# Performance work log

Hardware: AMD Instinct MI355X
Metric: run time of the kernel (lower is better)

## Reference

```python
import jax, jax.numpy as jnp
import numpy as np

N, DEG, F_IN, H = 50000, 16, 128, 32
E = N * DEG


def _linear_params(key, out_f, in_f):
    kw, kb = jax.random.split(key)
    s = 1.0 / np.sqrt(in_f)
    W = jax.random.uniform(kw, (out_f, in_f), jnp.float32, -s, s)
    b = jax.random.uniform(kb, (out_f,), jnp.float32, -s, s)
    return W, b


def setup_inputs() -> dict:
    key = jax.random.key(0)
    ks = jax.random.split(key, 12)
    X = jax.random.normal(ks[0], (N, F_IN), jnp.float32)
    # DEG distinct nonzero offsets shared by all rows -> unique (src,dst) pairs,
    # so the COO tensor is already coalesced (no duplicate indices).
    offsets = jax.random.permutation(ks[1], jnp.arange(1, N))[:DEG]
    src = jnp.repeat(jnp.arange(N, dtype=jnp.int32), DEG)
    dst = ((src.reshape(N, DEG) + offsets[None, :].astype(jnp.int32)) % N).reshape(-1)
    D = jax.ops.segment_sum(jnp.ones((E,), jnp.float32), src, num_segments=N)
    wn1p, bn1p = _linear_params(ks[2], H, F_IN)      # convN1.pass_map
    wn1s, bn1s = _linear_params(ks[3], H, F_IN)      # convN1.self_map
    we1p, be1p = _linear_params(ks[4], H, 2 * H)     # convE1.pass_map
    we1s, be1s = _linear_params(ks[5], H, F_IN)      # convE1.self_map
    wn2p, bn2p = _linear_params(ks[6], H, H)         # convN2.pass_map
    wn2s, bn2s = _linear_params(ks[7], H, H)         # convN2.self_map
    we2p, be2p = _linear_params(ks[8], H, 2 * H)     # convE2.pass_map
    we2s, be2s = _linear_params(ks[9], H, H)         # convE2.self_map
    wc, bc = _linear_params(ks[10], 1, H)            # classifier
    return dict(X=X, src=src, dst=dst, D=D,
                wn1p=wn1p, bn1p=bn1p, wn1s=wn1s, bn1s=bn1s,
                we1p=we1p, be1p=be1p, we1s=we1s, be1s=be1s,
                wn2p=wn2p, bn2p=bn2p, wn2s=wn2s, bn2s=bn2s,
                we2p=we2p, be2p=be2p, we2s=we2s, be2s=be2s,
                wc=wc, bc=bc)


def reference(X, src, dst, D,
              wn1p, bn1p, wn1s, bn1s,
              we1p, be1p, we1s, be1s,
              wn2p, bn2p, wn2s, bn2s,
              we2p, be2p, we2s, be2s,
              wc, bc):
    n = X.shape[0]

    def node_conv(vals, Xn, wp, bp, ws, bs):
        # torch.sparse.sum(A, dim=1): sum edge values per source row
        Asum = jax.ops.segment_sum(vals, src, num_segments=n)
        return jax.nn.relu((Asum / D[:, None]) @ wp.T + bp + Xn @ ws.T + bs)

    def edge_conv(vals, Xn, wp, bp, ws, bs):
        X1, X2 = Xn[src], Xn[dst]
        Ef = jnp.concatenate([(X1 - X2) * 0.5, (X1 + X2) * 0.5], axis=-1)
        return jax.nn.relu(Ef @ wp.T + bp + vals @ ws.T + bs)

    # add_graph: edge features = |X[src] - X[dst]|
    vals0 = jnp.abs(X[src] - X[dst])            # (E, F_IN)
    X0 = jnp.zeros_like(X)                       # forward zeros node features
    Xn1 = node_conv(vals0, X0, wn1p, bn1p, wn1s, bn1s)   # (N, 32)
    vals1 = edge_conv(vals0, Xn1, we1p, be1p, we1s, be1s)  # (E, 32)
    Xn2 = node_conv(vals1, Xn1, wn2p, bn2p, wn2s, bn2s)  # (N, 32)
    vals2 = edge_conv(vals1, Xn2, we2p, be2p, we2s, be2s)  # (E, 32)
    SX = jax.nn.sigmoid(vals2 @ wc.T + bc)[:, 0]          # (E,)
    return SX
```

## Files before the change

kernel.cpp:

```cpp
#include <hip/hip_runtime.h>

#define DEG 16
#define F_IN 128
#define H 32

typedef __attribute__((ext_vector_type(8))) _Float16 f16x8;
typedef __attribute__((ext_vector_type(4))) float f32x4;
typedef __attribute__((ext_vector_type(4))) int i32x4;
typedef __attribute__((ext_vector_type(4))) float fv4;
typedef __attribute__((ext_vector_type(2))) unsigned int uv2;

union HS  { _Float16 f; unsigned short s; };
union HF4 { _Float16 h[4]; uv2 u; };

__device__ __forceinline__ float relu_f(float x) { return fmaxf(x, 0.0f); }

__device__ __forceinline__ f16x8 habs8(f16x8 a) {
    union { f16x8 h; i32x4 i; } u; u.h = a;
#pragma unroll
    for (int k = 0; k < 4; ++k) u.i[k] &= 0x7FFF7FFF;
    return u.h;
}

__global__ __launch_bounds__(256) void k_pre(
    const float* __restrict__ X, _Float16* __restrict__ Xh, long n8,
    const float* __restrict__ we1s, const float* __restrict__ we1p,
    const float* __restrict__ be1p, const float* __restrict__ be1s,
    const float* __restrict__ we2p, const float* __restrict__ we2s,
    const float* __restrict__ be2p, const float* __restrict__ be2s,
    const float* __restrict__ wn1p, const float* __restrict__ bn1p,
    const float* __restrict__ bn1s,
    const float* __restrict__ wn2p, const float* __restrict__ bn2p,
    const float* __restrict__ wn2s, const float* __restrict__ bn2s,
    _Float16* __restrict__ Wcat1, _Float16* __restrict__ Wcat2,
    _Float16* __restrict__ Wn1ph,
    _Float16* __restrict__ Wn2ph, _Float16* __restrict__ Wn2sh,
    float* __restrict__ bias1, float* __restrict__ bias2,
    float* __restrict__ biasn1, float* __restrict__ biasn2)
{
    if (blockIdx.x >= 32) {
        const long t = (long)(blockIdx.x - 32) * 256 + threadIdx.x;
        if (t >= n8) return;
        const fv4* p = (const fv4*)X + t * 2;
        const fv4 a = __builtin_nontemporal_load(p);
        const fv4 b = __builtin_nontemporal_load(p + 1);
        f16x8 h;
        h[0] = (_Float16)a[0]; h[1] = (_Float16)a[1]; h[2] = (_Float16)a[2]; h[3] = (_Float16)a[3];
        h[4] = (_Float16)b[0]; h[5] = (_Float16)b[1]; h[6] = (_Float16)b[2]; h[7] = (_Float16)b[3];
        *(f16x8*)(Xh + t * 8) = h;
        return;
    }
    const int t0 = blockIdx.x * 256 + threadIdx.x;
    const int stride = 32 * 256;
    for (int idx = t0; idx < 32 * 192; idx += stride) {
        const int n = idx / 192, k = idx - n * 192;
        float w;
        if (k < 128)       w = we1s[n * 128 + k];
        else if (k < 160)  w = 0.5f * we1p[n * 64 + (k - 128)];
        else               w = 0.5f * we1p[n * 64 + 32 + (k - 160)];
        Wcat1[idx] = (_Float16)w;
    }
    for (int idx = t0; idx < 32 * 96; idx += stride) {
        const int n = idx / 96, k = idx - n * 96;
        float w;
        if (k < 32)       w = 0.5f * we2p[n * 64 + k];
        else if (k < 64)  w = 0.5f * we2p[n * 64 + 32 + (k - 32)];
        else              w = we2s[n * 32 + (k - 64)];
        Wcat2[idx] = (_Float16)w;
    }
    for (int idx = t0; idx < 32 * 128; idx += stride)
        Wn1ph[idx] = (_Float16)wn1p[idx];
    for (int idx = t0; idx < 32 * 32; idx += stride) {
        Wn2ph[idx] = (_Float16)wn2p[idx];
        Wn2sh[idx] = (_Float16)wn2s[idx];
    }
    if (t0 < H) {
        bias1[t0]  = be1p[t0] + be1s[t0];
        bias2[t0]  = be2p[t0] + be2s[t0];
        biasn1[t0] = bn1p[t0] + bn1s[t0];
        biasn2[t0] = bn2p[t0] + bn2s[t0];
    }
}

__global__ __launch_bounds__(64, 3) void k_p1(
    const _Float16* __restrict__ Xh, const int* __restrict__ dst,
    const float* __restrict__ D,
    const _Float16* __restrict__ Wcat1, const _Float16* __restrict__ Wn1ph,
    const float* __restrict__ biasn1,
    _Float16* __restrict__ t1h, _Float16* __restrict__ Xn1h, int N)
{
    const int lane = threadIdx.x;
    const int m = lane & 15, g = lane >> 4;
    const int i0 = blockIdx.x * 16;
    const int srow = (i0 + m < N) ? (i0 + m) : (N - 1);

    i32x4 dj4[4];
    {
        const i32x4* dp = (const i32x4*)(dst + (size_t)srow * DEG);
#pragma unroll
        for (int q = 0; q < 4; ++q) dj4[q] = dp[q];
    }
    f16x8 sv[4];
#pragma unroll
    for (int kb = 0; kb < 4; ++kb)
        sv[kb] = *(const f16x8*)(Xh + (size_t)srow * F_IN + kb * 32 + g * 8);
    f16x8 Bs[4][2], Bn[4][2];
#pragma unroll
    for (int kb = 0; kb < 4; ++kb)
#pragma unroll
        for (int t = 0; t < 2; ++t) {
            Bs[kb][t] = *(const f16x8*)(Wcat1 + (t * 16 + m) * 192 + kb * 32 + g * 8);
            Bn[kb][t] = *(const f16x8*)(Wn1ph + (t * 16 + m) * 128 + kb * 32 + g * 8);
        }

    f16x8 tvc[4], tvn[4];
#pragma unroll
    for (int kb = 0; kb < 4; ++kb)
        tvc[kb] = *(const f16x8*)(Xh + (size_t)dj4[0][0] * F_IN + kb * 32 + g * 8);

    f32x4 cn0 = {0.f,0.f,0.f,0.f}, cn1 = {0.f,0.f,0.f,0.f};
#pragma unroll
    for (int j = 0; j < 16; ++j) {
        if (j < 15) {
            const int dn = dj4[(j + 1) >> 2][(j + 1) & 3];
#pragma unroll
            for (int kb = 0; kb < 4; ++kb)
                tvn[kb] = *(const f16x8*)(Xh + (size_t)dn * F_IN + kb * 32 + g * 8);
        }
        f32x4 cs0 = {0.f,0.f,0.f,0.f}, cs1 = {0.f,0.f,0.f,0.f};
#pragma unroll
        for (int kb = 0; kb < 4; ++kb) {
            const f16x8 a = habs8(sv[kb] - tvc[kb]);
            cs0 = __builtin_amdgcn_mfma_f32_16x16x32_f16(a, Bs[kb][0], cs0, 0, 0, 0);
            cs1 = __builtin_amdgcn_mfma_f32_16x16x32_f16(a, Bs[kb][1], cs1, 0, 0, 0);
            cn0 = __builtin_amdgcn_mfma_f32_16x16x32_f16(a, Bn[kb][0], cn0, 0, 0, 0);
            cn1 = __builtin_amdgcn_mfma_f32_16x16x32_f16(a, Bn[kb][1], cn1, 0, 0, 0);
        }
        const size_t tb = ((size_t)blockIdx.x * 16 + j) * 512;
        HF4 a;
#pragma unroll
        for (int r = 0; r < 4; ++r) a.h[r] = (_Float16)cs0[r];
        __builtin_nontemporal_store(a.u, (uv2*)(t1h + tb + lane * 4));
#pragma unroll
        for (int r = 0; r < 4; ++r) a.h[r] = (_Float16)cs1[r];
        __builtin_nontemporal_store(a.u, (uv2*)(t1h + tb + 256 + lane * 4));
#pragma unroll
        for (int kb = 0; kb < 4; ++kb) tvc[kb] = tvn[kb];
    }
    const float bn0 = biasn1[m], bn1v = biasn1[16 + m];
#pragma unroll
    for (int r = 0; r < 4; ++r) {
        const int node = i0 + g * 4 + r;
        if (node < N) {
            const float invD = 1.0f / D[node];
            Xn1h[(size_t)node * H + m]      = (_Float16)relu_f(cn0[r] * invD + bn0);
            Xn1h[(size_t)node * H + 16 + m] = (_Float16)relu_f(cn1[r] * invD + bn1v);
        }
    }
}

__global__ __launch_bounds__(256, 4) void k_p2(
    const int* __restrict__ dst, const _Float16* __restrict__ Xn1h,
    const _Float16* __restrict__ Wcat1, const float* __restrict__ bias1,
    const _Float16* __restrict__ Wn2ph, const _Float16* __restrict__ Wn2sh,
    const float* __restrict__ biasn2, const float* __restrict__ D,
    _Float16* t1v1,
    _Float16* __restrict__ Xn2h, int N)
{
    __shared__ unsigned short RP[4][16 * 40];
    __shared__ float red[4][8][64];
    const int tid = threadIdx.x;
    const int lane = tid & 63;
    const int w = tid >> 6;
    const int m = lane & 15, g = lane >> 4;
    const int i0 = blockIdx.x * 16;
    const int srow = (i0 + m < N) ? (i0 + m) : (N - 1);

    const i32x4 dj = ((const i32x4*)(dst + (size_t)srow * DEG))[w];
    const f16x8 x1 = *(const f16x8*)(Xn1h + (size_t)srow * H + g * 8);
    f16x8 Bf[2][2];
#pragma unroll
    for (int kb = 0; kb < 2; ++kb)
#pragma unroll
        for (int t = 0; t < 2; ++t)
            Bf[kb][t] = *(const f16x8*)(Wcat1 + (t * 16 + m) * 192 + (4 + kb) * 32 + g * 8);

    f16x8 x2c, x2n;
    uv2 u0c, u1c, u0n, u1n;
    {
        const int d0 = dj[0];
        x2c = *(const f16x8*)(Xn1h + (size_t)d0 * H + g * 8);
        const size_t tb = ((size_t)blockIdx.x * 16 + w * 4) * 512;
        u0c = __builtin_nontemporal_load((const uv2*)(t1v1 + tb + lane * 4));
        u1c = __builtin_nontemporal_load((const uv2*)(t1v1 + tb + 256 + lane * 4));
    }
    const float b0 = bias1[m], b1v = bias1[16 + m];
    f32x4 sB0 = {0.f,0.f,0.f,0.f}, sB1 = {0.f,0.f,0.f,0.f};
    const int rr = lane >> 2, qq = lane & 3;
    unsigned short* RPw = RP[w];
#pragma unroll
    for (int jj = 0; jj < 4; ++jj) {
        if (jj < 3) {
            const int dn = dj[jj + 1];
            x2n = *(const f16x8*)(Xn1h + (size_t)dn * H + g * 8);
            const size_t tbn = ((size_t)blockIdx.x * 16 + w * 4 + jj + 1) * 512;
            u0n = __builtin_nontemporal_load((const uv2*)(t1v1 + tbn + lane * 4));
            u1n = __builtin_nontemporal_load((const uv2*)(t1v1 + tbn + 256 + lane * 4));
        }
        f32x4 c0, c1;
        { HF4 a; a.u = u0c;
#pragma unroll
          for (int r = 0; r < 4; ++r) c0[r] = (float)a.h[r];
          a.u = u1c;
#pragma unroll
          for (int r = 0; r < 4; ++r) c1[r] = (float)a.h[r]; }
        const f16x8 ad = x1 - x2c;
        const f16x8 aS = x1 + x2c;
        c0 = __builtin_amdgcn_mfma_f32_16x16x32_f16(ad, Bf[0][0], c0, 0, 0, 0);
        c1 = __builtin_amdgcn_mfma_f32_16x16x32_f16(ad, Bf[0][1], c1, 0, 0, 0);
        c0 = __builtin_amdgcn_mfma_f32_16x16x32_f16(aS, Bf[1][0], c0, 0, 0, 0);
        c1 = __builtin_amdgcn_mfma_f32_16x16x32_f16(aS, Bf[1][1], c1, 0, 0, 0);
#pragma unroll
        for (int r = 0; r < 4; ++r) {
            const float v0 = relu_f(c0[r] + b0);
            const float v1 = relu_f(c1[r] + b1v);
            HS h0, h1; h0.f = (_Float16)v0; h1.f = (_Float16)v1;
            RPw[(g * 4 + r) * 40 + m]      = h0.s;
            RPw[(g * 4 + r) * 40 + 16 + m] = h1.s;
            sB0[r] += v0; sB1[r] += v1;
        }
        const size_t tb = ((size_t)blockIdx.x * 16 + w * 4 + jj) * 512;
        const i32x4 v = *(const i32x4*)(RPw + rr * 40 + qq * 8);
        *(i32x4*)(t1v1 + tb + rr * 32 + qq * 8) = v;
        x2c = x2n; u0c = u0n; u1c = u1n;
    }
#pragma unroll
    for (int r = 0; r < 4; ++r) {
        red[w][r][lane]     = sB0[r];
        red[w][4 + r][lane] = sB1[r];
    }
    __syncthreads();
    if (w == 0) {
        _Float16* RPh = (_Float16*)RP[0];
#pragma unroll
        for (int r = 0; r < 4; ++r) {
            const int node = i0 + g * 4 + r;
            const float invD = 1.0f / D[(node < N) ? node : (N - 1)];
            const float a0 = red[0][r][lane] + red[1][r][lane]
                           + red[2][r][lane] + red[3][r][lane];
            const float a1 = red[0][4+r][lane] + red[1][4+r][lane]
                           + red[2][4+r][lane] + red[3][4+r][lane];
            RPh[(g * 4 + r) * 40 + m]      = (_Float16)(a0 * invD);
            RPh[(g * 4 + r) * 40 + 16 + m] = (_Float16)(a1 * invD);
        }
        const f16x8 aF = *(const f16x8*)(RPh + m * 40 + g * 8);
        f16x8 Bp[2], Bs2[2];
#pragma unroll
        for (int t = 0; t < 2; ++t) {
            Bp[t]  = *(const f16x8*)(Wn2ph + (t * 16 + m) * H + g * 8);
            Bs2[t] = *(const f16x8*)(Wn2sh + (t * 16 + m) * H + g * 8);
        }
        f32x4 c0 = {0.f,0.f,0.f,0.f}, c1 = {0.f,0.f,0.f,0.f};
        c0 = __builtin_amdgcn_mfma_f32_16x16x32_f16(aF, Bp[0], c0, 0, 0, 0);
        c1 = __builtin_amdgcn_mfma_f32_16x16x32_f16(aF, Bp[1], c1, 0, 0, 0);
        c0 = __builtin_amdgcn_mfma_f32_16x16x32_f16(x1, Bs2[0], c0, 0, 0, 0);
        c1 = __builtin_amdgcn_mfma_f32_16x16x32_f16(x1, Bs2[1], c1, 0, 0, 0);
        const float bp0 = biasn2[m], bp1 = biasn2[16 + m];
#pragma unroll
        for (int r = 0; r < 4; ++r) {
            const int node = i0 + g * 4 + r;
            if (node < N) {
                Xn2h[(size_t)node * H + m]      = (_Float16)relu_f(c0[r] + bp0);
                Xn2h[(size_t)node * H + 16 + m] = (_Float16)relu_f(c1[r] + bp1);
            }
        }
    }
}

__global__ __launch_bounds__(256, 4) void k_p3(
    const _Float16* __restrict__ Xn2h, const int* __restrict__ dst,
    const _Float16* __restrict__ vals1,
    const _Float16* __restrict__ Wcat2, const float* __restrict__ bias2,
    const float* __restrict__ wc, const float* __restrict__ bc,
    float* __restrict__ out, int N)
{
    __shared__ float outS[16 * 16];
    const int tid = threadIdx.x;
    const int lane = tid & 63;
    const int w = tid >> 6;
    const int m = lane & 15, g = lane >> 4;
    const int i0 = blockIdx.x * 16;
    const int srow = (i0 + m < N) ? (i0 + m) : (N - 1);

    const i32x4 dj = ((const i32x4*)(dst + (size_t)srow * DEG))[w];
    const f16x8 x1 = *(const f16x8*)(Xn2h + (size_t)srow * H + g * 8);
    f16x8 Bf[3][2];
#pragma unroll
    for (int kb = 0; kb < 3; ++kb)
#pragma unroll
        for (int t = 0; t < 2; ++t)
            Bf[kb][t] = *(const f16x8*)(Wcat2 + (t * 16 + m) * 96 + kb * 32 + g * 8);

    f16x8 x2b[2], avb[2];
#pragma unroll
    for (int s = 0; s < 2; ++s) {
        const int dn = dj[s];
        x2b[s] = *(const f16x8*)(Xn2h + (size_t)dn * H + g * 8);
        avb[s] = *(const f16x8*)(vals1 + ((size_t)blockIdx.x * 16 + w * 4 + s) * 512 + m * 32 + g * 8);
    }
    const float b0 = bias2[m], b1v = bias2[16 + m];
    const float w0 = wc[m], w1 = wc[16 + m];
#pragma unroll
    for (int jj = 0; jj < 4; ++jj) {
        const int s = jj & 1;
        const f16x8 x2 = x2b[s];
        const f16x8 av = avb[s];
        if (jj < 2) {
            const int dn = dj[jj + 2];
            x2b[s] = *(const f16x8*)(Xn2h + (size_t)dn * H + g * 8);
            avb[s] = *(const f16x8*)(vals1 + ((size_t)blockIdx.x * 16 + w * 4 + jj + 2) * 512 + m * 32 + g * 8);
        }
        const f16x8 ad = x1 - x2;
        const f16x8 aS = x1 + x2;
        f32x4 c0 = {0.f,0.f,0.f,0.f}, c1 = {0.f,0.f,0.f,0.f};
        c0 = __builtin_amdgcn_mfma_f32_16x16x32_f16(ad, Bf[0][0], c0, 0, 0, 0);
        c1 = __builtin_amdgcn_mfma_f32_16x16x32_f16(ad, Bf[0][1], c1, 0, 0, 0);
        c0 = __builtin_amdgcn_mfma_f32_16x16x32_f16(aS, Bf[1][0], c0, 0, 0, 0);
        c1 = __builtin_amdgcn_mfma_f32_16x16x32_f16(aS, Bf[1][1], c1, 0, 0, 0);
        c0 = __builtin_amdgcn_mfma_f32_16x16x32_f16(av, Bf[2][0], c0, 0, 0, 0);
        c1 = __builtin_amdgcn_mfma_f32_16x16x32_f16(av, Bf[2][1], c1, 0, 0, 0);

        float sr[4];
#pragma unroll
        for (int r = 0; r < 4; ++r)
            sr[r] = relu_f(c0[r] + b0) * w0 + relu_f(c1[r] + b1v) * w1;
#pragma unroll
        for (int mask = 1; mask < 16; mask <<= 1) {
#pragma unroll
            for (int r = 0; r < 4; ++r)
                sr[r] += __shfl_xor(sr[r], mask);
        }
        if (m == 0) {
#pragma unroll
            for (int r = 0; r < 4; ++r)
                outS[(g * 4 + r) * 16 + (w * 4 + jj)] = sr[r];
        }
    }
    __syncthreads();
    {
        const float bcv = bc[0];
        const float v = outS[tid];
        const float o = 1.0f / (1.0f + __expf(-(v + bcv)));
        if (i0 + 16 <= N || (i0 + (tid >> 4)) < N)
            out[(size_t)i0 * DEG + tid] = o;
    }
}

extern "C" void kernel_launch(void* const* d_in, const int* in_sizes, int n_in,
                              void* d_out, int out_size, void* d_ws, size_t ws_size,
                              hipStream_t stream)
{
    const float* X    = (const float*)d_in[0];
    const int*   dst  = (const int*)  d_in[2];
    const float* D    = (const float*)d_in[3];
    const float* wn1p = (const float*)d_in[4];
    const float* bn1p = (const float*)d_in[5];
    const float* bn1s = (const float*)d_in[7];
    const float* we1p = (const float*)d_in[8];
    const float* be1p = (const float*)d_in[9];
    const float* we1s = (const float*)d_in[10];
    const float* be1s = (const float*)d_in[11];
    const float* wn2p = (const float*)d_in[12];
    const float* bn2p = (const float*)d_in[13];
    const float* wn2s = (const float*)d_in[14];
    const float* bn2s = (const float*)d_in[15];
    const float* we2p = (const float*)d_in[16];
    const float* be2p = (const float*)d_in[17];
    const float* we2s = (const float*)d_in[18];
    const float* be2s = (const float*)d_in[19];
    const float* wc   = (const float*)d_in[20];
    const float* bc   = (const float*)d_in[21];

    const int N = in_sizes[3];
    const int nbW = (N + 15) / 16;
    const size_t Epad = (size_t)nbW * 16 * DEG;

    char* w = (char*)d_ws;
    _Float16* t1v1  = (_Float16*)w;  w += Epad * H * 2;
    _Float16* Xh    = (_Float16*)w;  w += (size_t)N * F_IN * 2;
    _Float16* Xn1h  = (_Float16*)w;  w += (size_t)N * H * 2;
    _Float16* Xn2h  = (_Float16*)w;  w += (size_t)N * H * 2;
    _Float16* Wcat1 = (_Float16*)w;  w += 32 * 192 * 2;
    _Float16* Wcat2 = (_Float16*)w;  w += 32 * 96 * 2;
    _Float16* Wn1ph = (_Float16*)w;  w += 32 * 128 * 2;
    _Float16* Wn2ph = (_Float16*)w;  w += 32 * 32 * 2;
    _Float16* Wn2sh = (_Float16*)w;  w += 32 * 32 * 2;
    float* bias1  = (float*)w;       w += H * 4;
    float* bias2  = (float*)w;       w += H * 4;
    float* biasn1 = (float*)w;       w += H * 4;
    float* biasn2 = (float*)w;       w += H * 4;
    float* outp = (float*)d_out;

    const long n8 = (long)N * F_IN / 8;
    const int nbX = (int)((n8 + 255) / 256);

    k_pre<<<nbX + 32, 256, 0, stream>>>(X, Xh, n8,
                                        we1s, we1p, be1p, be1s, we2p, we2s, be2p, be2s,
                                        wn1p, bn1p, bn1s, wn2p, bn2p, wn2s, bn2s,
                                        Wcat1, Wcat2, Wn1ph, Wn2ph, Wn2sh,
                                        bias1, bias2, biasn1, biasn2);
    k_p1<<<nbW, 64, 0, stream>>>(Xh, dst, D, Wcat1, Wn1ph, biasn1, t1v1, Xn1h, N);
    k_p2<<<nbW, 256, 0, stream>>>(dst, Xn1h, Wcat1, bias1, Wn2ph, Wn2sh,
                                  biasn2, D, t1v1, Xn2h, N);
    k_p3<<<nbW, 256, 0, stream>>>(Xn2h, dst, t1v1, Wcat2, bias2, wc, bc, outp, N);
}
```

Before: 196.1 us.

## Split k_p1 output columns across two wavefronts per block

```diff
diff --git a/kernel.cpp b/kernel.cpp
--- a/kernel.cpp
+++ b/kernel.cpp
@@ -82,14 +82,15 @@
     }
 }
 
-__global__ __launch_bounds__(64, 3) void k_p1(
+__global__ __launch_bounds__(128, 4) void k_p1(
     const _Float16* __restrict__ Xh, const int* __restrict__ dst,
     const float* __restrict__ D,
     const _Float16* __restrict__ Wcat1, const _Float16* __restrict__ Wn1ph,
     const float* __restrict__ biasn1,
     _Float16* __restrict__ t1h, _Float16* __restrict__ Xn1h, int N)
 {
-    const int lane = threadIdx.x;
+    const int lane = threadIdx.x & 63;
+    const int w = threadIdx.x >> 6;
     const int m = lane & 15, g = lane >> 4;
     const int i0 = blockIdx.x * 16;
     const int srow = (i0 + m < N) ? (i0 + m) : (N - 1);
@@ -104,21 +105,19 @@
 #pragma unroll
     for (int kb = 0; kb < 4; ++kb)
         sv[kb] = *(const f16x8*)(Xh + (size_t)srow * F_IN + kb * 32 + g * 8);
-    f16x8 Bs[4][2], Bn[4][2];
-#pragma unroll
-    for (int kb = 0; kb < 4; ++kb)
-#pragma unroll
-        for (int t = 0; t < 2; ++t) {
-            Bs[kb][t] = *(const f16x8*)(Wcat1 + (t * 16 + m) * 192 + kb * 32 + g * 8);
-            Bn[kb][t] = *(const f16x8*)(Wn1ph + (t * 16 + m) * 128 + kb * 32 + g * 8);
-        }
+    f16x8 Bs[4], Bn[4];
+#pragma unroll
+    for (int kb = 0; kb < 4; ++kb) {
+        Bs[kb] = *(const f16x8*)(Wcat1 + (w * 16 + m) * 192 + kb * 32 + g * 8);
+        Bn[kb] = *(const f16x8*)(Wn1ph + (w * 16 + m) * 128 + kb * 32 + g * 8);
+    }
 
     f16x8 tvc[4], tvn[4];
 #pragma unroll
     for (int kb = 0; kb < 4; ++kb)
         tvc[kb] = *(const f16x8*)(Xh + (size_t)dj4[0][0] * F_IN + kb * 32 + g * 8);
 
-    f32x4 cn0 = {0.f,0.f,0.f,0.f}, cn1 = {0.f,0.f,0.f,0.f};
+    f32x4 cn = {0.f,0.f,0.f,0.f};
 #pragma unroll
     for (int j = 0; j < 16; ++j) {
         if (j < 15) {
@@ -127,34 +126,28 @@
             for (int kb = 0; kb < 4; ++kb)
                 tvn[kb] = *(const f16x8*)(Xh + (size_t)dn * F_IN + kb * 32 + g * 8);
         }
-        f32x4 cs0 = {0.f,0.f,0.f,0.f}, cs1 = {0.f,0.f,0.f,0.f};
+        f32x4 cs = {0.f,0.f,0.f,0.f};
 #pragma unroll
         for (int kb = 0; kb < 4; ++kb) {
             const f16x8 a = habs8(sv[kb] - tvc[kb]);
-            cs0 = __builtin_amdgcn_mfma_f32_16x16x32_f16(a, Bs[kb][0], cs0, 0, 0, 0);
-            cs1 = __builtin_amdgcn_mfma_f32_16x16x32_f16(a, Bs[kb][1], cs1, 0, 0, 0);
-            cn0 = __builtin_amdgcn_mfma_f32_16x16x32_f16(a, Bn[kb][0], cn0, 0, 0, 0);
-            cn1 = __builtin_amdgcn_mfma_f32_16x16x32_f16(a, Bn[kb][1], cn1, 0, 0, 0);
+            cs = __builtin_amdgcn_mfma_f32_16x16x32_f16(a, Bs[kb], cs, 0, 0, 0);
+            cn = __builtin_amdgcn_mfma_f32_16x16x32_f16(a, Bn[kb], cn, 0, 0, 0);
         }
         const size_t tb = ((size_t)blockIdx.x * 16 + j) * 512;
-        HF4 a;
-#pragma unroll
-        for (int r = 0; r < 4; ++r) a.h[r] = (_Float16)cs0[r];
-        __builtin_nontemporal_store(a.u, (uv2*)(t1h + tb + lane * 4));
-#pragma unroll
-        for (int r = 0; r < 4; ++r) a.h[r] = (_Float16)cs1[r];
-        __builtin_nontemporal_store(a.u, (uv2*)(t1h + tb + 256 + lane * 4));
+        HF4 a4;
+#pragma unroll
+        for (int r = 0; r < 4; ++r) a4.h[r] = (_Float16)cs[r];
+        __builtin_nontemporal_store(a4.u, (uv2*)(t1h + tb + w * 256 + lane * 4));
 #pragma unroll
         for (int kb = 0; kb < 4; ++kb) tvc[kb] = tvn[kb];
     }
-    const float bn0 = biasn1[m], bn1v = biasn1[16 + m];
+    const float bn0 = biasn1[w * 16 + m];
 #pragma unroll
     for (int r = 0; r < 4; ++r) {
         const int node = i0 + g * 4 + r;
         if (node < N) {
             const float invD = 1.0f / D[node];
-            Xn1h[(size_t)node * H + m]      = (_Float16)relu_f(cn0[r] * invD + bn0);
-            Xn1h[(size_t)node * H + 16 + m] = (_Float16)relu_f(cn1[r] * invD + bn1v);
+            Xn1h[(size_t)node * H + w * 16 + m] = (_Float16)relu_f(cn[r] * invD + bn0);
         }
     }
 }
@@ -409,7 +402,7 @@
                                         wn1p, bn1p, bn1s, wn2p, bn2p, wn2s, bn2s,
                                         Wcat1, Wcat2, Wn1ph, Wn2ph, Wn2sh,
                                         bias1, bias2, biasn1, biasn2);
-    k_p1<<<nbW, 64, 0, stream>>>(Xh, dst, D, Wcat1, Wn1ph, biasn1, t1v1, Xn1h, N);
+    k_p1<<<nbW, 128, 0, stream>>>(Xh, dst, D, Wcat1, Wn1ph, biasn1, t1v1, Xn1h, N);
     k_p2<<<nbW, 256, 0, stream>>>(dst, Xn1h, Wcat1, bias1, Wn2ph, Wn2sh,
                                   biasn2, D, t1v1, Xn2h, N);
     k_p3<<<nbW, 256, 0, stream>>>(Xn2h, dst, t1v1, Wcat2, bias2, wc, bc, outp, N);
```

After: 215.6 us. 9.9% more time.
